# Performance work log

Measured on AMD Instinct MI355X. Metric: run time of the kernel, lower is better.

The kernel has to match this reference:

```python
import jax, jax.numpy as jnp
import numpy as np

DIM = 4096
N_HEADS = 32
N_KV_HEADS = 8
HEAD_DIM = DIM // N_HEADS  # 128
N_REP = N_HEADS // N_KV_HEADS  # 4
MAX_BS = 16
MAX_SEQ = 4096
SEQLEN = 1
START_POS = 4095
ROPE_THETA = 500000.0


def setup_inputs() -> dict:
    key = jax.random.key(0)
    ks = jax.random.split(key, 8)
    w_scale = 0.02  # keep logits in a sane range
    x = jax.random.normal(ks[0], (MAX_BS, SEQLEN, DIM), dtype=jnp.float32)
    wq = jax.random.normal(ks[1], (DIM, N_HEADS * HEAD_DIM), dtype=jnp.float32) * w_scale
    wk = jax.random.normal(ks[2], (DIM, N_KV_HEADS * HEAD_DIM), dtype=jnp.float32) * w_scale
    wv = jax.random.normal(ks[3], (DIM, N_KV_HEADS * HEAD_DIM), dtype=jnp.float32) * w_scale
    wo = jax.random.normal(ks[4], (N_HEADS * HEAD_DIM, DIM), dtype=jnp.float32) * w_scale
    cache_k = jax.random.normal(ks[5], (MAX_BS, MAX_SEQ, N_KV_HEADS, HEAD_DIM), dtype=jnp.float32)
    cache_v = jax.random.normal(ks[6], (MAX_BS, MAX_SEQ, N_KV_HEADS, HEAD_DIM), dtype=jnp.float32)
    # true rotary frequencies for positions [START_POS, START_POS+SEQLEN)
    inv_freq = 1.0 / (ROPE_THETA ** (np.arange(0, HEAD_DIM, 2, dtype=np.float32) / HEAD_DIM))  # [hd/2]
    t = np.arange(START_POS, START_POS + SEQLEN, dtype=np.float32)[:, None]  # [s,1]
    angles = t * inv_freq[None, :]  # [s, hd/2]
    freqs_cos = jnp.asarray(np.cos(angles), dtype=jnp.float32)
    freqs_sin = jnp.asarray(np.sin(angles), dtype=jnp.float32)
    return {"x": x, "wq": wq, "wk": wk, "wv": wv, "wo": wo,
            "cache_k": cache_k, "cache_v": cache_v,
            "freqs_cos": freqs_cos, "freqs_sin": freqs_sin,
            "start_pos": START_POS}


def _rope(t, cos, sin):
    # t: [b, s, h, hd]; cos/sin: [s, hd/2] -> broadcast [1, s, 1, hd/2]
    b, s, h, hd = t.shape
    tp = t.reshape(b, s, h, hd // 2, 2)
    e, o = tp[..., 0], tp[..., 1]
    c = cos[None, :, None, :]
    sn = sin[None, :, None, :]
    re = e * c - o * sn
    im = e * sn + o * c
    return jnp.stack([re, im], axis=-1).reshape(b, s, h, hd)


def reference(x, wq, wk, wv, wo, cache_k, cache_v, freqs_cos, freqs_sin, start_pos):
    bsz, seqlen, _ = x.shape
    xq = (x @ wq).reshape(bsz, seqlen, N_HEADS, HEAD_DIM)
    xk = (x @ wk).reshape(bsz, seqlen, N_KV_HEADS, HEAD_DIM)
    xv = (x @ wv).reshape(bsz, seqlen, N_KV_HEADS, HEAD_DIM)
    xq = _rope(xq, freqs_cos, freqs_sin)
    xk = _rope(xk, freqs_cos, freqs_sin)
    # KV-cache append
    cache_k = jax.lax.dynamic_update_slice(cache_k, xk, (0, start_pos, 0, 0))
    cache_v = jax.lax.dynamic_update_slice(cache_v, xv, (0, start_pos, 0, 0))
    kv_len = start_pos + seqlen  # static Python int
    keys = cache_k[:, :kv_len]    # [b, t, g, hd]
    values = cache_v[:, :kv_len]  # [b, t, g, hd]
    # GQA via broadcasting (math-equivalent to repeat_kv)
    q = xq.reshape(bsz, seqlen, N_KV_HEADS, N_REP, HEAD_DIM)
    scale = 1.0 / jnp.sqrt(jnp.float32(HEAD_DIM))
    scores = jnp.einsum('bsgrh,btgh->bgrst', q, keys) * scale  # [b,g,r,s,t]
    probs = jax.nn.softmax(scores.astype(jnp.float32), axis=-1).astype(xq.dtype)
    out = jnp.einsum('bgrst,btgh->bsgrh', probs, values)  # [b,s,g,r,hd]
    out = out.reshape(bsz, seqlen, N_HEADS * HEAD_DIM)
    return out @ wo
```

## Files before the change

### kernel.cpp

```cpp
#include <hip/hip_runtime.h>
#include <math.h>

#define DIM    4096
#define NH     32
#define NKV    8
#define HD     128
#define BS     16
#define KVLEN  4096
#define LASTPOS 4095
#define QKV_COLS 6144
#define CHUNK  256
#define NCH    16
#define SS_STR 264
#define NKC    64

#define WS_QKV   0
#define WS_ATTN  98304
#define WS_PART  163840
#define WS_PQ    1228800
#define WS_PW    7520256

__global__ __launch_bounds__(256) void qkv_projA(
    const float* __restrict__ x, const float* __restrict__ wq,
    const float* __restrict__ wk, const float* __restrict__ wv,
    float* __restrict__ pq) {
  __shared__ float xs[16 * 64];
  const int tid = threadIdx.x;
  const int col = (blockIdx.x * 256 + tid) * 2;
  const int kc = blockIdx.y;
  const int k0 = kc * 64;

  for (int i = tid; i < 1024; i += 256) {
    int b = i >> 6, k = i & 63;
    xs[i] = x[b * DIM + k0 + k];
  }
  __syncthreads();

  const float* w;
  int wstride, wcol;
  if (col < 4096)      { w = wq; wstride = 4096; wcol = col; }
  else if (col < 5120) { w = wk; wstride = 1024; wcol = col - 4096; }
  else                 { w = wv; wstride = 1024; wcol = col - 5120; }
  const float* wp = w + (size_t)k0 * wstride + wcol;

  float acc0[16], acc1[16];
#pragma unroll
  for (int b = 0; b < 16; ++b) { acc0[b] = 0.f; acc1[b] = 0.f; }

#pragma unroll 2
  for (int k = 0; k < 64; k += 4) {
    float2 w0 = *(const float2*)(wp + (size_t)(k + 0) * wstride);
    float2 w1 = *(const float2*)(wp + (size_t)(k + 1) * wstride);
    float2 w2 = *(const float2*)(wp + (size_t)(k + 2) * wstride);
    float2 w3 = *(const float2*)(wp + (size_t)(k + 3) * wstride);
#pragma unroll
    for (int b = 0; b < 16; ++b) {
      float4 xb = *(const float4*)(&xs[b * 64 + k]);
      acc0[b] += xb.x * w0.x + xb.y * w1.x + xb.z * w2.x + xb.w * w3.x;
      acc1[b] += xb.x * w0.y + xb.y * w1.y + xb.z * w2.y + xb.w * w3.y;
    }
  }
#pragma unroll
  for (int b = 0; b < 16; ++b) {
    *(float2*)(&pq[((size_t)kc * 16 + b) * QKV_COLS + col]) = make_float2(acc0[b], acc1[b]);
  }
}

__global__ __launch_bounds__(256) void qkv_projB(
    const float* __restrict__ pq, float* __restrict__ qkv,
    const float* __restrict__ fc, const float* __restrict__ fs) {
  int t = blockIdx.x * 256 + threadIdx.x;
  int b = t / 3072, pr = t % 3072;
  int col = 2 * pr;
  float e = 0.f, o = 0.f;
#pragma unroll 8
  for (int kc = 0; kc < NKC; ++kc) {
    float2 v = *(const float2*)(&pq[((size_t)kc * 16 + b) * QKV_COLS + col]);
    e += v.x; o += v.y;
  }
  float re = e, im = o;
  if (col < 5120) {
    int i = (col & 127) >> 1;
    float c = fc[i], s = fs[i];
    float scale = (col < 4096) ? 0.08838834764831845f : 1.0f;
    re = (e * c - o * s) * scale;
    im = (e * s + o * c) * scale;
  }
  *(float2*)(&qkv[b * QKV_COLS + col]) = make_float2(re, im);
}

__global__ __launch_bounds__(512, 8) void attn_partial(
    const float* __restrict__ cache_k, const float* __restrict__ cache_v,
    const float* __restrict__ qkv, float* __restrict__ part) {
  __shared__ float qs[512];
  __shared__ float ss[4 * SS_STR];
  __shared__ float pacc[8][4][128];
  const int tid = threadIdx.x;
  const int w = tid >> 6, lane = tid & 63;
  const int p = lane >> 4, ql = lane & 15;
  const int chunk = blockIdx.x & 15;
  const int bg = blockIdx.x >> 4;
  const int b = bg >> 3, g = bg & 7;

  qs[tid] = qkv[b * QKV_COLS + g * 512 + tid];
  __syncthreads();

  float4 qA[4], qB[4];
#pragma unroll
  for (int h = 0; h < 4; ++h) {
    qA[h] = *(const float4*)(&qs[h * 128 + ql * 8]);
    qB[h] = *(const float4*)(&qs[h * 128 + ql * 8 + 4]);
  }

  const int t0 = chunk * CHUNK;
  const float* kbase = cache_k + ((size_t)b * 4096 * 8 + g) * 128;
  const float* xk    = qkv + b * QKV_COLS + 4096 + g * 128;

#pragma unroll 1
  for (int it = 0; it < 8; ++it) {
    int r = w * 32 + it * 4 + p;
    int t = t0 + r;
    const float* krow = (t == LASTPOS) ? xk : (kbase + (size_t)t * 1024);
    float4 k0 = *(const float4*)(krow + ql * 8);
    float4 k1 = *(const float4*)(krow + ql * 8 + 4);
    float s[4];
#pragma unroll
    for (int h = 0; h < 4; ++h) {
      s[h] = k0.x * qA[h].x + k0.y * qA[h].y + k0.z * qA[h].z + k0.w * qA[h].w
           + k1.x * qB[h].x + k1.y * qB[h].y + k1.z * qB[h].z + k1.w * qB[h].w;
    }
#pragma unroll
    for (int off = 1; off < 16; off <<= 1) {
#pragma unroll
      for (int h = 0; h < 4; ++h) s[h] += __shfl_xor(s[h], off);
    }
    float v = (ql == 0) ? s[0] : (ql == 1) ? s[1] : (ql == 2) ? s[2] : s[3];
    if (ql < 4) ss[ql * SS_STR + r] = v;
  }
  __syncthreads();

  float* prow = part + ((size_t)(bg * NCH + chunk) * 4 + (w & 3)) * 130;
  if (w < 4) {
    float vals[4];
    float m = -1e30f;
#pragma unroll
    for (int i = 0; i < 4; ++i) {
      vals[i] = ss[w * SS_STR + lane + 64 * i];
      m = fmaxf(m, vals[i]);
    }
#pragma unroll
    for (int off = 1; off < 64; off <<= 1) m = fmaxf(m, __shfl_xor(m, off));
    float l = 0.f;
#pragma unroll
    for (int i = 0; i < 4; ++i) {
      float pe = __expf(vals[i] - m);
      ss[w * SS_STR + lane + 64 * i] = pe;
      l += pe;
    }
#pragma unroll
    for (int off = 1; off < 64; off <<= 1) l += __shfl_xor(l, off);
    if (lane == 0) { prow[128] = m; prow[129] = l; }
  }
  __syncthreads();

  const float* vbase = cache_v + ((size_t)b * 4096 * 8 + g) * 128;
  const float* xv    = qkv + b * QKV_COLS + 5120 + g * 128;
  const int h2 = lane >> 5;
  const int dq = lane & 31;
  float4 acc[4];
#pragma unroll
  for (int h = 0; h < 4; ++h) acc[h] = make_float4(0.f, 0.f, 0.f, 0.f);

#pragma unroll 4
  for (int j = 0; j < 16; ++j) {
    int r = w * 32 + 2 * j + h2;
    int t = t0 + r;
    const float* vrow = (t == LASTPOS) ? xv : (vbase + (size_t)t * 1024);
    float4 vv = *(const float4*)(vrow + dq * 4);
    float p0 = ss[0 * SS_STR + r];
    float p1 = ss[1 * SS_STR + r];
    float p2 = ss[2 * SS_STR + r];
    float p3 = ss[3 * SS_STR + r];
    acc[0].x += p0 * vv.x; acc[0].y += p0 * vv.y; acc[0].z += p0 * vv.z; acc[0].w += p0 * vv.w;
    acc[1].x += p1 * vv.x; acc[1].y += p1 * vv.y; acc[1].z += p1 * vv.z; acc[1].w += p1 * vv.w;
    acc[2].x += p2 * vv.x; acc[2].y += p2 * vv.y; acc[2].z += p2 * vv.z; acc[2].w += p2 * vv.w;
    acc[3].x += p3 * vv.x; acc[3].y += p3 * vv.y; acc[3].z += p3 * vv.z; acc[3].w += p3 * vv.w;
  }
#pragma unroll
  for (int h = 0; h < 4; ++h) {
    acc[h].x += __shfl_xor(acc[h].x, 32);
    acc[h].y += __shfl_xor(acc[h].y, 32);
    acc[h].z += __shfl_xor(acc[h].z, 32);
    acc[h].w += __shfl_xor(acc[h].w, 32);
  }
  if (lane < 32) {
#pragma unroll
    for (int h = 0; h < 4; ++h)
      *(float4*)(&pacc[w][h][dq * 4]) = acc[h];
  }
  __syncthreads();

  {
    int h = tid >> 7, d = tid & 127;
    float sum = 0.f;
#pragma unroll
    for (int w2 = 0; w2 < 8; ++w2) sum += pacc[w2][h][d];
    part[((size_t)(bg * NCH + chunk) * 4 + h) * 130 + d] = sum;
  }
}

__global__ __launch_bounds__(256) void attn_combine(
    const float* __restrict__ part, float* __restrict__ attn_out) {
  int t = blockIdx.x * 256 + threadIdx.x;
  int d = t & 127, r = (t >> 7) & 3, bg = t >> 9;
  int b = bg >> 3, g = bg & 7;
  float M = -1e30f;
  float ms[NCH];
#pragma unroll
  for (int c = 0; c < NCH; ++c) {
    ms[c] = part[((size_t)(bg * NCH + c) * 4 + r) * 130 + 128];
    M = fmaxf(M, ms[c]);
  }
  float num = 0.f, den = 0.f;
#pragma unroll
  for (int c = 0; c < NCH; ++c) {
    const float* prow = part + ((size_t)(bg * NCH + c) * 4 + r) * 130;
    float wgt = __expf(ms[c] - M);
    num += wgt * prow[d];
    den += wgt * prow[129];
  }
  attn_out[b * DIM + (g * 4 + r) * 128 + d] = num / den;
}

__global__ __launch_bounds__(256) void out_projA(
    const float* __restrict__ attn, const float* __restrict__ wo,
    float* __restrict__ pw) {
  __shared__ float xs[16 * 64];
  const int tid = threadIdx.x;
  const int col = (blockIdx.x * 256 + tid) * 2;
  const int kc = blockIdx.y;
  const int k0 = kc * 64;

  for (int i = tid; i < 1024; i += 256) {
    int b = i >> 6, k = i & 63;
    xs[i] = attn[b * DIM + k0 + k];
  }
  __syncthreads();

  const float* wp = wo + (size_t)k0 * 4096 + col;
  float acc0[16], acc1[16];
#pragma unroll
  for (int b = 0; b < 16; ++b) { acc0[b] = 0.f; acc1[b] = 0.f; }

#pragma unroll 2
  for (int k = 0; k < 64; k += 4) {
    float2 w0 = *(const float2*)(wp + (size_t)(k + 0) * 4096);
    float2 w1 = *(const float2*)(wp + (size_t)(k + 1) * 4096);
    float2 w2 = *(const float2*)(wp + (size_t)(k + 2) * 4096);
    float2 w3 = *(const float2*)(wp + (size_t)(k + 3) * 4096);
#pragma unroll
    for (int b = 0; b < 16; ++b) {
      float4 xb = *(const float4*)(&xs[b * 64 + k]);
      acc0[b] += xb.x * w0.x + xb.y * w1.x + xb.z * w2.x + xb.w * w3.x;
      acc1[b] += xb.x * w0.y + xb.y * w1.y + xb.z * w2.y + xb.w * w3.y;
    }
  }
#pragma unroll
  for (int b = 0; b < 16; ++b) {
    *(float2*)(&pw[((size_t)kc * 16 + b) * DIM + col]) = make_float2(acc0[b], acc1[b]);
  }
}

__global__ __launch_bounds__(256) void out_projB(
    const float* __restrict__ pw, float* __restrict__ out) {
  int t = blockIdx.x * 256 + threadIdx.x;
  int b = t >> 12, col = t & 4095;
  float sum = 0.f;
#pragma unroll 8
  for (int kc = 0; kc < NKC; ++kc)
    sum += pw[((size_t)kc * 16 + b) * DIM + col];
  out[b * DIM + col] = sum;
}

extern "C" void kernel_launch(void* const* d_in, const int* in_sizes, int n_in,
                              void* d_out, int out_size, void* d_ws, size_t ws_size,
                              hipStream_t stream) {
  const float* x  = (const float*)d_in[0];
  const float* wq = (const float*)d_in[1];
  const float* wk = (const float*)d_in[2];
  const float* wv = (const float*)d_in[3];
  const float* wo = (const float*)d_in[4];
  const float* ck = (const float*)d_in[5];
  const float* cv = (const float*)d_in[6];
  const float* fc = (const float*)d_in[7];
  const float* fs = (const float*)d_in[8];

  float* ws_f  = (float*)d_ws;
  float* qkv   = ws_f + WS_QKV;
  float* attn  = ws_f + WS_ATTN;
  float* part  = ws_f + WS_PART;
  float* pq    = ws_f + WS_PQ;
  float* pw    = ws_f + WS_PW;
  float* out   = (float*)d_out;

  qkv_projA<<<dim3(12, NKC), 256, 0, stream>>>(x, wq, wk, wv, pq);
  qkv_projB<<<192, 256, 0, stream>>>(pq, qkv, fc, fs);
  attn_partial<<<2048, 512, 0, stream>>>(ck, cv, qkv, part);
  attn_combine<<<256, 256, 0, stream>>>(part, attn);
  out_projA<<<dim3(8, NKC), 256, 0, stream>>>(attn, wo, pw);
  out_projB<<<256, 256, 0, stream>>>(pw, out);
}
```

Baseline: 185.4 us.

## Make attention partials per-wave without LDS and add two-level combine

The attention partial kernel now gives each 64-lane wave an independent 32-token unit. Softmax max and sum stay in registers and probabilities are broadcast with shuffles, so shared memory and block barriers are gone. K/V cache loads use nontemporal loads. Because this produces 128 partials per (batch, group) instead of 16, a two-stage combine kernel is added, which costs an extra launch and more partial-buffer traffic.

Result: slower. 194.6 us (+5.0%).

```diff
diff --git a/kernel.cpp b/kernel.cpp
--- a/kernel.cpp
+++ b/kernel.cpp
@@ -9,16 +9,20 @@
 #define KVLEN  4096
 #define LASTPOS 4095
 #define QKV_COLS 6144
-#define CHUNK  256
-#define NCH    16
-#define SS_STR 264
 #define NKC    64
+
+typedef float f32x4 __attribute__((ext_vector_type(4)));
+
+__device__ __forceinline__ f32x4 ntload4(const float* p) {
+  return __builtin_nontemporal_load((const f32x4*)p);
+}
 
 #define WS_QKV   0
 #define WS_ATTN  98304
 #define WS_PART  163840
-#define WS_PQ    1228800
-#define WS_PW    7520256
+#define WS_PART2 8814592
+#define WS_PQ    9084928
+#define WS_PW    15376384
 
 __global__ __launch_bounds__(256) void qkv_projA(
     const float* __restrict__ x, const float* __restrict__ wq,
@@ -89,147 +93,160 @@
   *(float2*)(&qkv[b * QKV_COLS + col]) = make_float2(re, im);
 }
 
-__global__ __launch_bounds__(512, 8) void attn_partial(
+__global__ __launch_bounds__(256, 4) void attn_partial(
     const float* __restrict__ cache_k, const float* __restrict__ cache_v,
     const float* __restrict__ qkv, float* __restrict__ part) {
-  __shared__ float qs[512];
-  __shared__ float ss[4 * SS_STR];
-  __shared__ float pacc[8][4][128];
   const int tid = threadIdx.x;
   const int w = tid >> 6, lane = tid & 63;
   const int p = lane >> 4, ql = lane & 15;
-  const int chunk = blockIdx.x & 15;
-  const int bg = blockIdx.x >> 4;
+  const int chunk = blockIdx.x & 31;
+  const int bg = blockIdx.x >> 5;
   const int b = bg >> 3, g = bg & 7;
-
-  qs[tid] = qkv[b * QKV_COLS + g * 512 + tid];
-  __syncthreads();
-
-  float4 qA[4], qB[4];
+  const int unit = chunk * 4 + w;
+  const int t0w = chunk * 128 + w * 32;
+
+  const float* qbase = qkv + b * QKV_COLS + g * 512;
+  f32x4 qA[4], qB[4];
 #pragma unroll
   for (int h = 0; h < 4; ++h) {
-    qA[h] = *(const float4*)(&qs[h * 128 + ql * 8]);
-    qB[h] = *(const float4*)(&qs[h * 128 + ql * 8 + 4]);
-  }
-
-  const int t0 = chunk * CHUNK;
+    qA[h] = *(const f32x4*)(qbase + h * 128 + ql * 8);
+    qB[h] = *(const f32x4*)(qbase + h * 128 + ql * 8 + 4);
+  }
+
   const float* kbase = cache_k + ((size_t)b * 4096 * 8 + g) * 128;
   const float* xk    = qkv + b * QKV_COLS + 4096 + g * 128;
 
-#pragma unroll 1
+  float sv8[8];
+#pragma unroll
   for (int it = 0; it < 8; ++it) {
-    int r = w * 32 + it * 4 + p;
-    int t = t0 + r;
+    int t = t0w + it * 4 + p;
     const float* krow = (t == LASTPOS) ? xk : (kbase + (size_t)t * 1024);
-    float4 k0 = *(const float4*)(krow + ql * 8);
-    float4 k1 = *(const float4*)(krow + ql * 8 + 4);
+    f32x4 k0 = ntload4(krow + ql * 8);
+    f32x4 k1 = ntload4(krow + ql * 8 + 4);
     float s[4];
 #pragma unroll
     for (int h = 0; h < 4; ++h) {
-      s[h] = k0.x * qA[h].x + k0.y * qA[h].y + k0.z * qA[h].z + k0.w * qA[h].w
-           + k1.x * qB[h].x + k1.y * qB[h].y + k1.z * qB[h].z + k1.w * qB[h].w;
+      s[h] = k0[0]*qA[h][0] + k0[1]*qA[h][1] + k0[2]*qA[h][2] + k0[3]*qA[h][3]
+           + k1[0]*qB[h][0] + k1[1]*qB[h][1] + k1[2]*qB[h][2] + k1[3]*qB[h][3];
     }
 #pragma unroll
     for (int off = 1; off < 16; off <<= 1) {
 #pragma unroll
       for (int h = 0; h < 4; ++h) s[h] += __shfl_xor(s[h], off);
     }
-    float v = (ql == 0) ? s[0] : (ql == 1) ? s[1] : (ql == 2) ? s[2] : s[3];
-    if (ql < 4) ss[ql * SS_STR + r] = v;
-  }
-  __syncthreads();
-
-  float* prow = part + ((size_t)(bg * NCH + chunk) * 4 + (w & 3)) * 130;
-  if (w < 4) {
-    float vals[4];
-    float m = -1e30f;
-#pragma unroll
-    for (int i = 0; i < 4; ++i) {
-      vals[i] = ss[w * SS_STR + lane + 64 * i];
-      m = fmaxf(m, vals[i]);
-    }
-#pragma unroll
-    for (int off = 1; off < 64; off <<= 1) m = fmaxf(m, __shfl_xor(m, off));
-    float l = 0.f;
-#pragma unroll
-    for (int i = 0; i < 4; ++i) {
-      float pe = __expf(vals[i] - m);
-      ss[w * SS_STR + lane + 64 * i] = pe;
-      l += pe;
-    }
-#pragma unroll
-    for (int off = 1; off < 64; off <<= 1) l += __shfl_xor(l, off);
-    if (lane == 0) { prow[128] = m; prow[129] = l; }
-  }
-  __syncthreads();
+    int hsel = ql & 3;
+    float v = s[0];
+    if (hsel == 1) v = s[1];
+    if (hsel == 2) v = s[2];
+    if (hsel == 3) v = s[3];
+    sv8[it] = v;
+  }
+
+  float m = -1e30f;
+#pragma unroll
+  for (int it = 0; it < 8; ++it) m = fmaxf(m, sv8[it]);
+  m = fmaxf(m, __shfl_xor(m, 16));
+  m = fmaxf(m, __shfl_xor(m, 32));
+  float l = 0.f;
+#pragma unroll
+  for (int it = 0; it < 8; ++it) { sv8[it] = __expf(sv8[it] - m); l += sv8[it]; }
+  l += __shfl_xor(l, 16);
+  l += __shfl_xor(l, 32);
+  if (lane < 4) {
+    size_t pi = ((size_t)(bg * 128 + unit) * 4 + lane) * 132;
+    part[pi + 128] = m;
+    part[pi + 129] = l;
+  }
 
   const float* vbase = cache_v + ((size_t)b * 4096 * 8 + g) * 128;
   const float* xv    = qkv + b * QKV_COLS + 5120 + g * 128;
   const int h2 = lane >> 5;
   const int dq = lane & 31;
-  float4 acc[4];
-#pragma unroll
-  for (int h = 0; h < 4; ++h) acc[h] = make_float4(0.f, 0.f, 0.f, 0.f);
-
+  f32x4 acc[4];
+#pragma unroll
+  for (int h = 0; h < 4; ++h) acc[h] = (f32x4)(0.f);
+
+#pragma unroll
+  for (int jj = 0; jj < 16; ++jj) {
+    int lr = 2 * jj + h2;
+    int t = t0w + lr;
+    const float* vrow = (t == LASTPOS) ? xv : (vbase + (size_t)t * 1024);
+    f32x4 vv = ntload4(vrow + dq * 4);
+    float sreg = sv8[jj >> 1];
+    int srcb = (lr & 3) << 4;
+    float p0 = __shfl(sreg, srcb + 0);
+    float p1 = __shfl(sreg, srcb + 1);
+    float p2 = __shfl(sreg, srcb + 2);
+    float p3 = __shfl(sreg, srcb + 3);
+    acc[0] += p0 * vv;
+    acc[1] += p1 * vv;
+    acc[2] += p2 * vv;
+    acc[3] += p3 * vv;
+  }
+#pragma unroll
+  for (int h = 0; h < 4; ++h) {
+    acc[h][0] += __shfl_xor(acc[h][0], 32);
+    acc[h][1] += __shfl_xor(acc[h][1], 32);
+    acc[h][2] += __shfl_xor(acc[h][2], 32);
+    acc[h][3] += __shfl_xor(acc[h][3], 32);
+  }
+  if (lane < 32) {
+#pragma unroll
+    for (int h = 0; h < 4; ++h) {
+      size_t pi = ((size_t)(bg * 128 + unit) * 4 + h) * 132;
+      *(f32x4*)(&part[pi + dq * 4]) = acc[h];
+    }
+  }
+}
+
+__global__ __launch_bounds__(512) void attn_combine1(
+    const float* __restrict__ part, float* __restrict__ part2) {
+  const int bgs = blockIdx.x;
+  const int bg = bgs >> 2, s = bgs & 3;
+  const int tid = threadIdx.x;
+  __shared__ float ml[32][4][2];
+  for (int i = tid; i < 256; i += 512) {
+    int u = i >> 3, h = (i >> 1) & 3, q = i & 1;
+    ml[u][h][q] = part[((size_t)(bg * 128 + s * 32 + u) * 4 + h) * 132 + 128 + q];
+  }
+  __syncthreads();
+  const int h = tid >> 7, d = tid & 127;
+  float M = -1e30f;
+#pragma unroll
+  for (int u = 0; u < 32; ++u) M = fmaxf(M, ml[u][h][0]);
+  float num = 0.f, den = 0.f;
 #pragma unroll 4
-  for (int j = 0; j < 16; ++j) {
-    int r = w * 32 + 2 * j + h2;
-    int t = t0 + r;
-    const float* vrow = (t == LASTPOS) ? xv : (vbase + (size_t)t * 1024);
-    float4 vv = *(const float4*)(vrow + dq * 4);
-    float p0 = ss[0 * SS_STR + r];
-    float p1 = ss[1 * SS_STR + r];
-    float p2 = ss[2 * SS_STR + r];
-    float p3 = ss[3 * SS_STR + r];
-    acc[0].x += p0 * vv.x; acc[0].y += p0 * vv.y; acc[0].z += p0 * vv.z; acc[0].w += p0 * vv.w;
-    acc[1].x += p1 * vv.x; acc[1].y += p1 * vv.y; acc[1].z += p1 * vv.z; acc[1].w += p1 * vv.w;
-    acc[2].x += p2 * vv.x; acc[2].y += p2 * vv.y; acc[2].z += p2 * vv.z; acc[2].w += p2 * vv.w;
-    acc[3].x += p3 * vv.x; acc[3].y += p3 * vv.y; acc[3].z += p3 * vv.z; acc[3].w += p3 * vv.w;
-  }
-#pragma unroll
-  for (int h = 0; h < 4; ++h) {
-    acc[h].x += __shfl_xor(acc[h].x, 32);
-    acc[h].y += __shfl_xor(acc[h].y, 32);
-    acc[h].z += __shfl_xor(acc[h].z, 32);
-    acc[h].w += __shfl_xor(acc[h].w, 32);
-  }
-  if (lane < 32) {
-#pragma unroll
-    for (int h = 0; h < 4; ++h)
-      *(float4*)(&pacc[w][h][dq * 4]) = acc[h];
-  }
-  __syncthreads();
-
-  {
-    int h = tid >> 7, d = tid & 127;
-    float sum = 0.f;
-#pragma unroll
-    for (int w2 = 0; w2 < 8; ++w2) sum += pacc[w2][h][d];
-    part[((size_t)(bg * NCH + chunk) * 4 + h) * 130 + d] = sum;
-  }
-}
-
-__global__ __launch_bounds__(256) void attn_combine(
-    const float* __restrict__ part, float* __restrict__ attn_out) {
+  for (int u = 0; u < 32; ++u) {
+    float wgt = __expf(ml[u][h][0] - M);
+    num += wgt * part[((size_t)(bg * 128 + s * 32 + u) * 4 + h) * 132 + d];
+    den += wgt * ml[u][h][1];
+  }
+  size_t po = ((size_t)bgs * 4 + h) * 132;
+  part2[po + d] = num;
+  if (d == 0) { part2[po + 128] = M; part2[po + 129] = den; }
+}
+
+__global__ __launch_bounds__(256) void attn_combine2(
+    const float* __restrict__ part2, float* __restrict__ attn_out) {
   int t = blockIdx.x * 256 + threadIdx.x;
-  int d = t & 127, r = (t >> 7) & 3, bg = t >> 9;
+  int d = t & 127, h = (t >> 7) & 3, bg = t >> 9;
   int b = bg >> 3, g = bg & 7;
+  float ms[4];
   float M = -1e30f;
-  float ms[NCH];
-#pragma unroll
-  for (int c = 0; c < NCH; ++c) {
-    ms[c] = part[((size_t)(bg * NCH + c) * 4 + r) * 130 + 128];
-    M = fmaxf(M, ms[c]);
+#pragma unroll
+  for (int s = 0; s < 4; ++s) {
+    ms[s] = part2[((size_t)(bg * 4 + s) * 4 + h) * 132 + 128];
+    M = fmaxf(M, ms[s]);
   }
   float num = 0.f, den = 0.f;
 #pragma unroll
-  for (int c = 0; c < NCH; ++c) {
-    const float* prow = part + ((size_t)(bg * NCH + c) * 4 + r) * 130;
-    float wgt = __expf(ms[c] - M);
-    num += wgt * prow[d];
-    den += wgt * prow[129];
-  }
-  attn_out[b * DIM + (g * 4 + r) * 128 + d] = num / den;
+  for (int s = 0; s < 4; ++s) {
+    const float* pr = part2 + ((size_t)(bg * 4 + s) * 4 + h) * 132;
+    float wgt = __expf(ms[s] - M);
+    num += wgt * pr[d];
+    den += wgt * pr[129];
+  }
+  attn_out[b * DIM + (g * 4 + h) * 128 + d] = num / den;
 }
 
 __global__ __launch_bounds__(256) void out_projA(
@@ -299,14 +316,16 @@
   float* qkv   = ws_f + WS_QKV;
   float* attn  = ws_f + WS_ATTN;
   float* part  = ws_f + WS_PART;
+  float* part2 = ws_f + WS_PART2;
   float* pq    = ws_f + WS_PQ;
   float* pw    = ws_f + WS_PW;
   float* out   = (float*)d_out;
 
   qkv_projA<<<dim3(12, NKC), 256, 0, stream>>>(x, wq, wk, wv, pq);
   qkv_projB<<<192, 256, 0, stream>>>(pq, qkv, fc, fs);
-  attn_partial<<<2048, 512, 0, stream>>>(ck, cv, qkv, part);
-  attn_combine<<<256, 256, 0, stream>>>(part, attn);
+  attn_partial<<<4096, 256, 0, stream>>>(ck, cv, qkv, part);
+  attn_combine1<<<512, 512, 0, stream>>>(part, part2);
+  attn_combine2<<<256, 256, 0, stream>>>(part2, attn);
   out_projA<<<dim3(8, NKC), 256, 0, stream>>>(attn, wo, pw);
   out_projB<<<256, 256, 0, stream>>>(pw, out);
 }
```
